# Kernel tuning notes

Measured on AMD Instinct MI355X. Metric: run time of the kernel, lower is better.

The kernel has to match this reference:

```python
import jax, jax.numpy as jnp
import numpy as np

D = 128   # embedding_dim
H = 256   # hidden_dim

def setup_inputs() -> dict:
    key = jax.random.key(0)
    ks = jax.random.split(key, 16)
    s = 0.02
    B, N = 4, 384
    inp = {
        "cities": jax.random.uniform(ks[0], (B, N, 2), dtype=jnp.float32),
        # city_encoder: Linear(2,H) -> ReLU -> Linear(H,D); weights stored [in,out]
        "We1": jax.random.normal(ks[1], (2, H), dtype=jnp.float32) * s,
        "be1": jnp.zeros((H,), jnp.float32),
        "We2": jax.random.normal(ks[2], (H, D), dtype=jnp.float32) * s,
        "be2": jnp.zeros((D,), jnp.float32),
        # attention: Linear(D,H) -> ReLU -> Linear(H,1)
        "Wa1": jax.random.normal(ks[3], (D, H), dtype=jnp.float32) * s,
        "ba1": jnp.zeros((H,), jnp.float32),
        "wa2": jax.random.normal(ks[4], (H, 1), dtype=jnp.float32) * s,
        "ba2": jnp.zeros((1,), jnp.float32),
        # decoder: Linear(2D,H) -> ReLU -> Linear(H,1) -> Sigmoid
        "Wd1": jax.random.normal(ks[5], (2 * D, H), dtype=jnp.float32) * s,
        "bd1": jnp.zeros((H,), jnp.float32),
        "wd2": jax.random.normal(ks[6], (H, 1), dtype=jnp.float32) * s,
        "bd2": jnp.zeros((1,), jnp.float32),
    }
    return inp


def reference(cities, We1, be1, We2, be2, Wa1, ba1, wa2, ba2, Wd1, bd1, wd2, bd2):
    B, N, _ = cities.shape
    # city encoder MLP: [B,N,2] -> [B,N,D]
    emb = jax.nn.relu(cities @ We1 + be1) @ We2 + be2
    # attention scores -> softmax over cities
    att = jax.nn.softmax((jax.nn.relu(emb @ Wa1 + ba1) @ wa2 + ba2).squeeze(-1), axis=1)
    # Pairwise decoder: concat(e_i, e_j) @ Wd1 == e_i @ Wd1[:D] + e_j @ Wd1[D:]
    Ai = emb @ Wd1[:D]   # [B,N,H] contribution of row city i
    Aj = emb @ Wd1[D:]   # [B,N,H] contribution of col city j
    h = jax.nn.relu(Ai[:, :, None, :] + Aj[:, None, :, :] + bd1)  # [B,N,N,H]
    p = jax.nn.sigmoid((h @ wd2).squeeze(-1) + bd2)               # [B,N,N]
    # diagonal (i == j) was never written in the torch loop -> stays 0
    p = p * (1.0 - jnp.eye(N, dtype=p.dtype))
    return att, p
```

## Files before the change

kernel.cpp:

```cpp
#include <hip/hip_runtime.h>
#include <hip/hip_fp16.h>
#include <math.h>

#define NCITY 384
#define BATCH 4
#define DIM   128
#define HID   256
#define M_TOT (BATCH * NCITY)
#define TR    6

#define HALF_FLOATS 16384

#define VMWAIT16() do { asm volatile("s_waitcnt vmcnt(16)" ::: "memory"); \
                        __builtin_amdgcn_sched_barrier(0); } while (0)
#define VMWAIT0()  do { asm volatile("s_waitcnt vmcnt(0)"  ::: "memory"); \
                        __builtin_amdgcn_sched_barrier(0); } while (0)
#define LGKM0()    do { asm volatile("s_waitcnt lgkmcnt(0)" ::: "memory"); \
                        __builtin_amdgcn_sched_barrier(0); } while (0)
#define SBAR()     do { __builtin_amdgcn_s_barrier(); \
                        __builtin_amdgcn_sched_barrier(0); } while (0)

__device__ __forceinline__ void stage64(const float* __restrict__ gsrc,
                                        float* lbuf, int tid)
{
    const int lane = tid & 63;
    const int wv   = tid >> 6;
    #pragma unroll
    for (int i = 0; i < 16; ++i) {
        const int slot = i * 4 + wv;
        __builtin_amdgcn_global_load_lds(
            (const __attribute__((address_space(1))) void*)(gsrc + slot * 256 + lane * 4),
            (__attribute__((address_space(3))) void*)(lbuf + slot * 256),
            16, 0, 0);
    }
}

__device__ __forceinline__ void emb_half(const float* buf,
                                         const float (*h1_s)[HID],
                                         int tid, int kbase, float4 eacc[TR])
{
    const int d4 = tid & 31;
    const int k0 = (tid >> 5) * 16;
    #pragma unroll 2
    for (int kb = 0; kb < 16; kb += 4) {
        float4 hv[TR];
        #pragma unroll
        for (int rr = 0; rr < TR; ++rr)
            hv[rr] = *(const float4*)&h1_s[rr][kbase + k0 + kb];
        #pragma unroll
        for (int kk = 0; kk < 4; ++kk) {
            const float4 w4 = *(const float4*)&buf[(k0 + kb + kk) * DIM + d4 * 4];
            #pragma unroll
            for (int rr = 0; rr < TR; ++rr) {
                const float h = ((const float*)&hv[rr])[kk];
                eacc[rr].x = fmaf(h, w4.x, eacc[rr].x);
                eacc[rr].y = fmaf(h, w4.y, eacc[rr].y);
                eacc[rr].z = fmaf(h, w4.z, eacc[rr].z);
                eacc[rr].w = fmaf(h, w4.w, eacc[rr].w);
            }
        }
    }
}

__device__ __forceinline__ void chunk_half(const float* buf,
                                           const float (*emb_s)[DIM],
                                           int tid, int kbase, float4 cacc[TR])
{
    const int c4 = tid & 63;
    const int k0 = (tid >> 6) * 16;
    #pragma unroll 2
    for (int kb = 0; kb < 16; kb += 4) {
        float4 ev[TR];
        #pragma unroll
        for (int rr = 0; rr < TR; ++rr)
            ev[rr] = *(const float4*)&emb_s[rr][kbase + k0 + kb];
        #pragma unroll
        for (int kk = 0; kk < 4; ++kk) {
            const float4 w4 = *(const float4*)&buf[(k0 + kb + kk) * HID + c4 * 4];
            #pragma unroll
            for (int rr = 0; rr < TR; ++rr) {
                const float e = ((const float*)&ev[rr])[kk];
                cacc[rr].x = fmaf(e, w4.x, cacc[rr].x);
                cacc[rr].y = fmaf(e, w4.y, cacc[rr].y);
                cacc[rr].z = fmaf(e, w4.z, cacc[rr].z);
                cacc[rr].w = fmaf(e, w4.w, cacc[rr].w);
            }
        }
    }
}

__device__ __forceinline__ void chunk_reduce(float* scr, int tid,
                                             const float4 cacc[TR], float out6[TR])
{
    const int c4 = tid & 63;
    const int wv = tid >> 6;
    SBAR();
    #pragma unroll
    for (int rr = 0; rr < TR; ++rr)
        *(float4*)&scr[(wv * TR + rr) * HID + c4 * 4] = cacc[rr];
    LGKM0(); SBAR();
    #pragma unroll
    for (int rr = 0; rr < TR; ++rr)
        out6[rr] = scr[(0 * TR + rr) * HID + tid] + scr[(1 * TR + rr) * HID + tid]
                 + scr[(2 * TR + rr) * HID + tid] + scr[(3 * TR + rr) * HID + tid];
}

__global__ __launch_bounds__(256) void encoder_kernel(
    const float* __restrict__ cities,
    const float* __restrict__ We1, const float* __restrict__ be1,
    const float* __restrict__ We2, const float* __restrict__ be2,
    const float* __restrict__ Wa1, const float* __restrict__ ba1,
    const float* __restrict__ wa2, const float* __restrict__ ba2,
    const float* __restrict__ Wd1, const float* __restrict__ bd1,
    float* __restrict__ score, float* __restrict__ Ai, float* __restrict__ Aj)
{
    __shared__ float wbuf[2 * HALF_FLOATS];
    __shared__ float h1_s[TR][HID];
    __shared__ float emb_s[TR][DIM];
    __shared__ float red2[4][TR];

    float* b0 = wbuf;
    float* b1 = wbuf + HALF_FLOATS;

    const int tid = threadIdx.x;
    const int r0  = blockIdx.x * TR;

    const float w0 = We1[tid], w1 = We1[HID + tid], bb1 = be1[tid];
    const float ba1v = ba1[tid], wa2v = wa2[tid], bd1v = bd1[tid];
    const float be2v = be2[tid & (DIM - 1)];
    float cx[TR], cy[TR];
    #pragma unroll
    for (int rr = 0; rr < TR; ++rr) {
        cx[rr] = cities[(r0 + rr) * 2];
        cy[rr] = cities[(r0 + rr) * 2 + 1];
    }
    #pragma unroll
    for (int rr = 0; rr < TR; ++rr)
        h1_s[rr][tid] = fmaxf(fmaf(cx[rr], w0, fmaf(cy[rr], w1, bb1)), 0.f);
    __builtin_amdgcn_sched_barrier(0);

    stage64(We2,               b0, tid);
    stage64(We2 + HALF_FLOATS, b1, tid);
    VMWAIT16(); LGKM0(); SBAR();

    float4 eacc[TR];
    #pragma unroll
    for (int rr = 0; rr < TR; ++rr) eacc[rr] = make_float4(0.f, 0.f, 0.f, 0.f);

    emb_half(b0, h1_s, tid, 0, eacc);
    SBAR();
    stage64(Wa1, b0, tid);
    VMWAIT16(); SBAR();
    emb_half(b1, h1_s, tid, 128, eacc);

    {
        #pragma unroll
        for (int rr = 0; rr < TR; ++rr) {
            eacc[rr].x += __shfl_xor(eacc[rr].x, 32);
            eacc[rr].y += __shfl_xor(eacc[rr].y, 32);
            eacc[rr].z += __shfl_xor(eacc[rr].z, 32);
            eacc[rr].w += __shfl_xor(eacc[rr].w, 32);
        }
        SBAR();
        if ((tid & 63) < 32) {
            const int wv = tid >> 6, d4 = tid & 31;
            #pragma unroll
            for (int rr = 0; rr < TR; ++rr)
                *(float4*)&b1[(wv * TR + rr) * DIM + d4 * 4] = eacc[rr];
        }
        LGKM0(); SBAR();
        #pragma unroll
        for (int j = 0; j < 3; ++j) {
            const int o = tid + j * 256;
            const int rr = o >> 7, d = o & (DIM - 1);
            emb_s[rr][d] = b1[(0 * TR + rr) * DIM + d] + b1[(1 * TR + rr) * DIM + d]
                         + b1[(2 * TR + rr) * DIM + d] + b1[(3 * TR + rr) * DIM + d]
                         + be2v;
        }
        LGKM0(); SBAR();
    }

    float4 cacc[TR];
    float o6[TR];

    stage64(Wa1 + HALF_FLOATS, b1, tid);
    VMWAIT16(); SBAR();
    #pragma unroll
    for (int rr = 0; rr < TR; ++rr) cacc[rr] = make_float4(0.f, 0.f, 0.f, 0.f);
    chunk_half(b0, emb_s, tid, 0, cacc);
    SBAR();
    stage64(Wd1, b0, tid);
    VMWAIT16(); SBAR();
    chunk_half(b1, emb_s, tid, 64, cacc);
    chunk_reduce(b1, tid, cacc, o6);
    {
        const int wv = tid >> 6;
        #pragma unroll
        for (int rr = 0; rr < TR; ++rr) {
            float v = fmaxf(o6[rr] + ba1v, 0.f) * wa2v;
            #pragma unroll
            for (int off = 32; off > 0; off >>= 1)
                v += __shfl_down(v, off);
            if ((tid & 63) == 0) red2[wv][rr] = v;
        }
        LGKM0(); SBAR();
        if (tid < TR)
            score[r0 + tid] = red2[0][tid] + red2[1][tid] + red2[2][tid] + red2[3][tid];
        SBAR();
    }

    stage64(Wd1 + HALF_FLOATS, b1, tid);
    VMWAIT16(); SBAR();
    #pragma unroll
    for (int rr = 0; rr < TR; ++rr) cacc[rr] = make_float4(0.f, 0.f, 0.f, 0.f);
    chunk_half(b0, emb_s, tid, 0, cacc);
    SBAR();
    stage64(Wd1 + 2 * HALF_FLOATS, b0, tid);
    VMWAIT16(); SBAR();
    chunk_half(b1, emb_s, tid, 64, cacc);
    chunk_reduce(b1, tid, cacc, o6);
    #pragma unroll
    for (int rr = 0; rr < TR; ++rr)
        Ai[(r0 + rr) * HID + tid] = o6[rr] + bd1v;
    SBAR();

    stage64(Wd1 + 3 * HALF_FLOATS, b1, tid);
    VMWAIT16(); SBAR();
    #pragma unroll
    for (int rr = 0; rr < TR; ++rr) cacc[rr] = make_float4(0.f, 0.f, 0.f, 0.f);
    chunk_half(b0, emb_s, tid, 0, cacc);
    VMWAIT0(); SBAR();
    chunk_half(b1, emb_s, tid, 64, cacc);
    chunk_reduce(b0, tid, cacc, o6);
    #pragma unroll
    for (int rr = 0; rr < TR; ++rr)
        Aj[(r0 + rr) * HID + tid] = o6[rr];
    (void)ba2;
}

__device__ __forceinline__ unsigned pk_add(unsigned a, unsigned b) {
    unsigned r;
    asm("v_pk_add_f16 %0, %1, %2" : "=v"(r) : "v"(a), "v"(b));
    return r;
}
__device__ __forceinline__ unsigned pk_max0(unsigned a) {
    unsigned r;
    asm("v_pk_max_f16 %0, %1, %2" : "=v"(r) : "v"(a), "v"(0u));
    return r;
}
__device__ __forceinline__ unsigned pk_fma(unsigned a, unsigned b, unsigned c) {
    unsigned r;
    asm("v_pk_fma_f16 %0, %1, %2, %3" : "=v"(r) : "v"(a), "v"(b), "v"(c));
    return r;
}
__device__ __forceinline__ unsigned pack2(float a, float b) {
    union { __half2 h2; unsigned u; } c;
    c.h2 = __float22half2_rn(make_float2(a, b));
    return c.u;
}
__device__ __forceinline__ float sum2(unsigned u) {
    union { unsigned u; __half2 h2; } c;
    c.u = u;
    return __low2float(c.h2) + __high2float(c.h2);
}

union H8 { float4 f4; unsigned u[4]; };

__global__ __launch_bounds__(256) void pair_sm_kernel(
    const float* __restrict__ Ai, const float* __restrict__ Aj,
    const float* __restrict__ wd2, const float* __restrict__ bd2,
    const float* __restrict__ score, float* __restrict__ att,
    float* __restrict__ p)
{
    const int tid = threadIdx.x;
    const int b   = blockIdx.y;

    if (blockIdx.x == 144) {
        __shared__ float red[8];
        const int t = tid;
        const float v0 = score[b * NCITY + t];
        const bool  h2v = (t < NCITY - 256);
        const float v1 = h2v ? score[b * NCITY + 256 + t] : -3.4e38f;
        float m = fmaxf(v0, v1);
        #pragma unroll
        for (int off = 32; off > 0; off >>= 1)
            m = fmaxf(m, __shfl_down(m, off));
        if ((t & 63) == 0) red[t >> 6] = m;
        __syncthreads();
        m = fmaxf(fmaxf(red[0], red[1]), fmaxf(red[2], red[3]));
        const float e0 = __expf(v0 - m);
        const float e1 = h2v ? __expf(v1 - m) : 0.f;
        float s = e0 + e1;
        #pragma unroll
        for (int off = 32; off > 0; off >>= 1)
            s += __shfl_down(s, off);
        if ((t & 63) == 0) red[4 + (t >> 6)] = s;
        __syncthreads();
        s = red[4] + red[5] + red[6] + red[7];
        att[b * NCITY + t] = e0 / s;
        if (h2v) att[b * NCITY + 256 + t] = e1 / s;
        return;
    }

    __shared__ __half ai_s[32 * HID];
    __shared__ __half aj_s[32 * HID];
    __shared__ unsigned wd2h[HID / 2];

    const int i0 = (blockIdx.x / 12) * 32;
    const int j0 = (blockIdx.x % 12) * 32;

    if (tid < HID / 2) {
        const float2 w2 = *(const float2*)&wd2[tid * 2];
        wd2h[tid] = pack2(w2.x, w2.y);
    }

    for (int u = tid; u < 32 * 32; u += 256) {
        const int r = u >> 5, s = u & 31;
        const int su = (s ^ (r & 15)) * 8;
        {
            const int g = (b * NCITY + i0 + r) * HID + s * 8;
            const float4 f0 = *(const float4*)&Ai[g];
            const float4 f1 = *(const float4*)&Ai[g + 4];
            H8 pk;
            pk.u[0] = pack2(f0.x, f0.y);
            pk.u[1] = pack2(f0.z, f0.w);
            pk.u[2] = pack2(f1.x, f1.y);
            pk.u[3] = pack2(f1.z, f1.w);
            *(float4*)&ai_s[r * HID + su] = pk.f4;
        }
        {
            const int g = (b * NCITY + j0 + r) * HID + s * 8;
            const float4 f0 = *(const float4*)&Aj[g];
            const float4 f1 = *(const float4*)&Aj[g + 4];
            H8 pk;
            pk.u[0] = pack2(f0.x, f0.y);
            pk.u[1] = pack2(f0.z, f0.w);
            pk.u[2] = pack2(f1.x, f1.y);
            pk.u[3] = pack2(f1.z, f1.w);
            *(float4*)&aj_s[r * HID + su] = pk.f4;
        }
    }
    __syncthreads();

    const int tx = tid & 15;
    const int ty = tid >> 4;

    unsigned a00A = 0u, a00B = 0u, a01A = 0u, a01B = 0u;
    unsigned a10A = 0u, a10B = 0u, a11A = 0u, a11B = 0u;

    #pragma unroll 4
    for (int k8 = 0; k8 < 32; ++k8) {
        const int ci = (k8 ^ ty) * 8;
        const int cj = (k8 ^ tx) * 8;
        H8 x0, x1, y0, y1;
        x0.f4 = *(const float4*)&ai_s[ ty       * HID + ci];
        x1.f4 = *(const float4*)&ai_s[(ty + 16) * HID + ci];
        y0.f4 = *(const float4*)&aj_s[ tx       * HID + cj];
        y1.f4 = *(const float4*)&aj_s[(tx + 16) * HID + cj];

        #pragma unroll
        for (int q = 0; q < 4; ++q) {
            const unsigned w = wd2h[k8 * 4 + q];
            const unsigned t00 = pk_max0(pk_add(x0.u[q], y0.u[q]));
            const unsigned t01 = pk_max0(pk_add(x0.u[q], y1.u[q]));
            const unsigned t10 = pk_max0(pk_add(x1.u[q], y0.u[q]));
            const unsigned t11 = pk_max0(pk_add(x1.u[q], y1.u[q]));
            if (q < 2) {
                a00A = pk_fma(t00, w, a00A);
                a01A = pk_fma(t01, w, a01A);
                a10A = pk_fma(t10, w, a10A);
                a11A = pk_fma(t11, w, a11A);
            } else {
                a00B = pk_fma(t00, w, a00B);
                a01B = pk_fma(t01, w, a01B);
                a10B = pk_fma(t10, w, a10B);
                a11B = pk_fma(t11, w, a11B);
            }
        }
    }

    const float bd = bd2[0];
    float accs[2][2];
    accs[0][0] = sum2(a00A) + sum2(a00B);
    accs[0][1] = sum2(a01A) + sum2(a01B);
    accs[1][0] = sum2(a10A) + sum2(a10B);
    accs[1][1] = sum2(a11A) + sum2(a11B);

    #pragma unroll
    for (int ii = 0; ii < 2; ++ii) {
        #pragma unroll
        for (int jj = 0; jj < 2; ++jj) {
            const int gi = i0 + ty + ii * 16;
            const int gj = j0 + tx + jj * 16;
            const float v = 1.f / (1.f + __expf(-(accs[ii][jj] + bd)));
            p[(b * NCITY + gi) * NCITY + gj] = (gi == gj) ? 0.f : v;
        }
    }
}

extern "C" void kernel_launch(void* const* d_in, const int* in_sizes, int n_in,
                              void* d_out, int out_size, void* d_ws, size_t ws_size,
                              hipStream_t stream)
{
    const float* cities = (const float*)d_in[0];
    const float* We1    = (const float*)d_in[1];
    const float* be1    = (const float*)d_in[2];
    const float* We2    = (const float*)d_in[3];
    const float* be2    = (const float*)d_in[4];
    const float* Wa1    = (const float*)d_in[5];
    const float* ba1    = (const float*)d_in[6];
    const float* wa2    = (const float*)d_in[7];
    const float* ba2    = (const float*)d_in[8];
    const float* Wd1    = (const float*)d_in[9];
    const float* bd1    = (const float*)d_in[10];
    const float* wd2    = (const float*)d_in[11];
    const float* bd2    = (const float*)d_in[12];

    float* out_att = (float*)d_out;
    float* out_p   = out_att + BATCH * NCITY;

    float* score = (float*)d_ws;
    float* Ai    = score + M_TOT;
    float* Aj    = Ai + M_TOT * HID;

    encoder_kernel<<<M_TOT / TR, 256, 0, stream>>>(
        cities, We1, be1, We2, be2, Wa1, ba1, wa2, ba2, Wd1, bd1,
        score, Ai, Aj);

    pair_sm_kernel<<<dim3(145, BATCH), 256, 0, stream>>>(
        Ai, Aj, wd2, bd2, score, out_att, out_p);
}
```

Measured before the change: 38.36 us.

## Halve rows per block and stage weights in smaller double-buffered chunks

Rows per block in the encoder/projection kernel drop from 6 to 3, doubling the grid, and each weight half-tile shrinks from 64 to 32 KB. The double-buffered LDS pipeline now runs through twice as many smaller stages with matching vmcnt waits. The goal is more blocks across CUs and a smaller LDS footprint for better occupancy. The cost is twice the total weight traffic across blocks and more barriers per block.

```diff
diff --git a/kernel.cpp b/kernel.cpp
--- a/kernel.cpp
+++ b/kernel.cpp
@@ -7,11 +7,11 @@
 #define DIM   128
 #define HID   256
 #define M_TOT (BATCH * NCITY)
-#define TR    6
-
-#define HALF_FLOATS 16384
-
-#define VMWAIT16() do { asm volatile("s_waitcnt vmcnt(16)" ::: "memory"); \
+#define TR    3
+
+#define HALF_FLOATS 8192
+
+#define VMWAIT8()  do { asm volatile("s_waitcnt vmcnt(8)"  ::: "memory"); \
                         __builtin_amdgcn_sched_barrier(0); } while (0)
 #define VMWAIT0()  do { asm volatile("s_waitcnt vmcnt(0)"  ::: "memory"); \
                         __builtin_amdgcn_sched_barrier(0); } while (0)
@@ -20,13 +20,13 @@
 #define SBAR()     do { __builtin_amdgcn_s_barrier(); \
                         __builtin_amdgcn_sched_barrier(0); } while (0)
 
-__device__ __forceinline__ void stage64(const float* __restrict__ gsrc,
+__device__ __forceinline__ void stage32(const float* __restrict__ gsrc,
                                         float* lbuf, int tid)
 {
     const int lane = tid & 63;
     const int wv   = tid >> 6;
     #pragma unroll
-    for (int i = 0; i < 16; ++i) {
+    for (int i = 0; i < 8; ++i) {
         const int slot = i * 4 + wv;
         __builtin_amdgcn_global_load_lds(
             (const __attribute__((address_space(1))) void*)(gsrc + slot * 256 + lane * 4),
@@ -40,9 +40,9 @@
                                          int tid, int kbase, float4 eacc[TR])
 {
     const int d4 = tid & 31;
-    const int k0 = (tid >> 5) * 16;
-    #pragma unroll 2
-    for (int kb = 0; kb < 16; kb += 4) {
+    const int k0 = (tid >> 5) * 8;
+    #pragma unroll
+    for (int kb = 0; kb < 8; kb += 4) {
         float4 hv[TR];
         #pragma unroll
         for (int rr = 0; rr < TR; ++rr)
@@ -67,9 +67,9 @@
                                            int tid, int kbase, float4 cacc[TR])
 {
     const int c4 = tid & 63;
-    const int k0 = (tid >> 6) * 16;
-    #pragma unroll 2
-    for (int kb = 0; kb < 16; kb += 4) {
+    const int k0 = (tid >> 6) * 8;
+    #pragma unroll
+    for (int kb = 0; kb < 8; kb += 4) {
         float4 ev[TR];
         #pragma unroll
         for (int rr = 0; rr < TR; ++rr)
@@ -139,19 +139,26 @@
         h1_s[rr][tid] = fmaxf(fmaf(cx[rr], w0, fmaf(cy[rr], w1, bb1)), 0.f);
     __builtin_amdgcn_sched_barrier(0);
 
-    stage64(We2,               b0, tid);
-    stage64(We2 + HALF_FLOATS, b1, tid);
-    VMWAIT16(); LGKM0(); SBAR();
-
     float4 eacc[TR];
     #pragma unroll
     for (int rr = 0; rr < TR; ++rr) eacc[rr] = make_float4(0.f, 0.f, 0.f, 0.f);
 
+    stage32(We2,                   b0, tid);
+    stage32(We2 + 1 * HALF_FLOATS, b1, tid);
+    VMWAIT8(); LGKM0(); SBAR();
     emb_half(b0, h1_s, tid, 0, eacc);
     SBAR();
-    stage64(Wa1, b0, tid);
-    VMWAIT16(); SBAR();
-    emb_half(b1, h1_s, tid, 128, eacc);
+    stage32(We2 + 2 * HALF_FLOATS, b0, tid);
+    VMWAIT8(); SBAR();
+    emb_half(b1, h1_s, tid, 64, eacc);
+    SBAR();
+    stage32(We2 + 3 * HALF_FLOATS, b1, tid);
+    VMWAIT8(); SBAR();
+    emb_half(b0, h1_s, tid, 128, eacc);
+    SBAR();
+    stage32(Wa1, b0, tid);
+    VMWAIT8(); SBAR();
+    emb_half(b1, h1_s, tid, 192, eacc);
 
     {
         #pragma unroll
@@ -170,12 +177,14 @@
         }
         LGKM0(); SBAR();
         #pragma unroll
-        for (int j = 0; j < 3; ++j) {
+        for (int j = 0; j < 2; ++j) {
             const int o = tid + j * 256;
-            const int rr = o >> 7, d = o & (DIM - 1);
-            emb_s[rr][d] = b1[(0 * TR + rr) * DIM + d] + b1[(1 * TR + rr) * DIM + d]
-                         + b1[(2 * TR + rr) * DIM + d] + b1[(3 * TR + rr) * DIM + d]
-                         + be2v;
+            if (o < TR * DIM) {
+                const int rr = o >> 7, d = o & (DIM - 1);
+                emb_s[rr][d] = b1[(0 * TR + rr) * DIM + d] + b1[(1 * TR + rr) * DIM + d]
+                             + b1[(2 * TR + rr) * DIM + d] + b1[(3 * TR + rr) * DIM + d]
+                             + be2v;
+            }
         }
         LGKM0(); SBAR();
     }
@@ -183,15 +192,23 @@
     float4 cacc[TR];
     float o6[TR];
 
-    stage64(Wa1 + HALF_FLOATS, b1, tid);
-    VMWAIT16(); SBAR();
+    stage32(Wa1 + 1 * HALF_FLOATS, b1, tid);
+    VMWAIT8(); SBAR();
     #pragma unroll
     for (int rr = 0; rr < TR; ++rr) cacc[rr] = make_float4(0.f, 0.f, 0.f, 0.f);
     chunk_half(b0, emb_s, tid, 0, cacc);
     SBAR();
-    stage64(Wd1, b0, tid);
-    VMWAIT16(); SBAR();
-    chunk_half(b1, emb_s, tid, 64, cacc);
+    stage32(Wa1 + 2 * HALF_FLOATS, b0, tid);
+    VMWAIT8(); SBAR();
+    chunk_half(b1, emb_s, tid, 32, cacc);
+    SBAR();
+    stage32(Wa1 + 3 * HALF_FLOATS, b1, tid);
+    VMWAIT8(); SBAR();
+    chunk_half(b0, emb_s, tid, 64, cacc);
+    SBAR();
+    stage32(Wd1, b0, tid);
+    VMWAIT8(); SBAR();
+    chunk_half(b1, emb_s, tid, 96, cacc);
     chunk_reduce(b1, tid, cacc, o6);
     {
         const int wv = tid >> 6;
@@ -206,31 +223,46 @@
         LGKM0(); SBAR();
         if (tid < TR)
             score[r0 + tid] = red2[0][tid] + red2[1][tid] + red2[2][tid] + red2[3][tid];
-        SBAR();
-    }
-
-    stage64(Wd1 + HALF_FLOATS, b1, tid);
-    VMWAIT16(); SBAR();
+    }
+
+    stage32(Wd1 + 1 * HALF_FLOATS, b1, tid);
+    VMWAIT8(); SBAR();
     #pragma unroll
     for (int rr = 0; rr < TR; ++rr) cacc[rr] = make_float4(0.f, 0.f, 0.f, 0.f);
     chunk_half(b0, emb_s, tid, 0, cacc);
     SBAR();
-    stage64(Wd1 + 2 * HALF_FLOATS, b0, tid);
-    VMWAIT16(); SBAR();
-    chunk_half(b1, emb_s, tid, 64, cacc);
+    stage32(Wd1 + 2 * HALF_FLOATS, b0, tid);
+    VMWAIT8(); SBAR();
+    chunk_half(b1, emb_s, tid, 32, cacc);
+    SBAR();
+    stage32(Wd1 + 3 * HALF_FLOATS, b1, tid);
+    VMWAIT8(); SBAR();
+    chunk_half(b0, emb_s, tid, 64, cacc);
+    SBAR();
+    stage32(Wd1 + 4 * HALF_FLOATS, b0, tid);
+    VMWAIT8(); SBAR();
+    chunk_half(b1, emb_s, tid, 96, cacc);
     chunk_reduce(b1, tid, cacc, o6);
     #pragma unroll
     for (int rr = 0; rr < TR; ++rr)
         Ai[(r0 + rr) * HID + tid] = o6[rr] + bd1v;
     SBAR();
 
-    stage64(Wd1 + 3 * HALF_FLOATS, b1, tid);
-    VMWAIT16(); SBAR();
+    stage32(Wd1 + 5 * HALF_FLOATS, b1, tid);
+    VMWAIT8(); SBAR();
     #pragma unroll
     for (int rr = 0; rr < TR; ++rr) cacc[rr] = make_float4(0.f, 0.f, 0.f, 0.f);
     chunk_half(b0, emb_s, tid, 0, cacc);
+    SBAR();
+    stage32(Wd1 + 6 * HALF_FLOATS, b0, tid);
+    VMWAIT8(); SBAR();
+    chunk_half(b1, emb_s, tid, 32, cacc);
+    SBAR();
+    stage32(Wd1 + 7 * HALF_FLOATS, b1, tid);
+    VMWAIT8(); SBAR();
+    chunk_half(b0, emb_s, tid, 64, cacc);
     VMWAIT0(); SBAR();
-    chunk_half(b1, emb_s, tid, 64, cacc);
+    chunk_half(b1, emb_s, tid, 96, cacc);
     chunk_reduce(b0, tid, cacc, o6);
     #pragma unroll
     for (int rr = 0; rr < TR; ++rr)
```

Measured after the change: 37.92 us. About the same (-1.2%).
